# Performance work log

Hardware: AMD Instinct MI355X
Metric: run time of the kernel (lower is better)

The kernel has to match this reference:

```python
import jax, jax.numpy as jnp
import numpy as np

G, N, F, H, L, B = 8, 1024, 128, 256, 4, 64


def setup_inputs() -> dict:
    key = jax.random.key(0)
    ks = jax.random.split(key, 8)
    graph = jax.random.randint(ks[0], (B,), 0, G)
    # boolean coverpoint mask; force column 0 True so no row is empty
    mask = jax.random.uniform(ks[1], (B, N)) < 0.2
    mask = mask.at[:, 0].set(True)
    cdfg_xs = jax.random.normal(ks[2], (G, N, F), dtype=jnp.float32)
    cdfg_as = (jax.random.uniform(ks[3], (G, N, N)) < 0.02).astype(jnp.float32) / 20.0
    W_in = jax.random.normal(ks[4], (F, H), dtype=jnp.float32) * (1.0 / np.sqrt(F))
    b_in = jnp.zeros((H,), dtype=jnp.float32)
    Ws = jax.random.normal(ks[5], (L, H, H), dtype=jnp.float32) * (1.0 / np.sqrt(H))
    bs = jnp.zeros((L, H), dtype=jnp.float32)
    return {"graph": graph, "coverpoint_mask": mask, "cdfg_xs": cdfg_xs,
            "cdfg_as": cdfg_as, "W_in": W_in, "b_in": b_in, "Ws": Ws, "bs": bs}


def reference(graph, coverpoint_mask, cdfg_xs, cdfg_as, W_in, b_in, Ws, bs):
    # gather per-sample graphs (tf.gather_nd equivalent)
    xs = cdfg_xs[graph]          # [B, N, F]
    As = cdfg_as[graph]          # [B, N, N]
    # input Dense with relu
    x = jax.nn.relu(jnp.einsum('bnf,fh->bnh', xs, W_in) + b_in)  # [B, N, H]
    to_add = x
    n_layers = Ws.shape[0]
    for i in range(n_layers):
        h = jnp.einsum('bnm,bmh->bnh', As, jnp.einsum('bnh,hk->bnk', x, Ws[i])) + bs[i]
        if i == n_layers - 1:
            x = jax.nn.softmax(h, axis=-1)   # final_activation='softmax'
        else:
            x = jax.nn.relu(h)
    x = x + to_add
    # ragged boolean_mask + reduce_mean over nodes == masked mean
    m = coverpoint_mask[..., None].astype(x.dtype)   # [B, N, 1]
    s = jnp.sum(x * m, axis=1)                       # [B, H]
    cnt = jnp.maximum(jnp.sum(m, axis=1), 1.0)
    return s / cnt
```

## Files before the change

kernel.cpp:

```cpp
#include <hip/hip_runtime.h>
#include <hip/hip_bf16.h>

#define GG 8
#define NN 1024
#define FF 128
#define HH 256
#define LL 4
#define BB 64
#define MM (GG * NN)
#define ELLCAP 96

typedef __attribute__((ext_vector_type(8))) short bf16x8_t;
typedef __attribute__((ext_vector_type(4))) float f32x4_t;

__device__ inline unsigned short f2bf(float f) {
  union { float f; unsigned u; } c;
  c.f = f;
  unsigned r = (c.u + 0x7fffu + ((c.u >> 16) & 1u)) >> 16;
  return (unsigned short)r;
}
__device__ inline float bf2f(unsigned short u) {
  union { unsigned u; float f; } c;
  c.u = (unsigned)u << 16;
  return c.f;
}

__global__ void detect_mask_kernel(const uint4* __restrict__ mb,
                                   int* __restrict__ flags) {
  const int i = blockIdx.x * blockDim.x + threadIdx.x;
  const uint4 v = mb[i];
  const unsigned all = v.x | v.y | v.z | v.w;
  const int nonz = (all & 0xFFFFFF00u) != 0;
  const int isf32 = ((v.x >> 24) == 0x3fu) || ((v.y >> 24) == 0x3fu) ||
                    ((v.z >> 24) == 0x3fu) || ((v.w >> 24) == 0x3fu);
  const unsigned long long bn = __ballot(nonz);
  const unsigned long long bf = __ballot(isf32);
  if ((threadIdx.x & 63) == 0) {
    if (bn) atomicOr(&flags[0], 1);
    if (bf) atomicOr(&flags[1], 1);
  }
}

__global__ __launch_bounds__(256) void convert_xs_kernel(
    const float4* __restrict__ in, ushort4* __restrict__ out) {
  const int i = blockIdx.x * 256 + threadIdx.x;
  const float4 v = in[i];
  ushort4 o;
  o.x = f2bf(v.x); o.y = f2bf(v.y); o.z = f2bf(v.z); o.w = f2bf(v.w);
  out[i] = o;
}

__global__ __launch_bounds__(256) void convert_w_kernel(
    const float* __restrict__ W_in, const float* __restrict__ Ws,
    unsigned short* __restrict__ WinT, unsigned short* __restrict__ WsT) {
  const int idx = blockIdx.x * 256 + threadIdx.x;
  if (idx < FF * HH) {
    const int n = idx >> 7, k = idx & (FF - 1);
    WinT[idx] = f2bf(W_in[k * HH + n]);
  } else {
    const int j = idx - FF * HH;
    const int l = j >> 16, n = (j >> 8) & 255, k = j & 255;
    WsT[j] = f2bf(Ws[((size_t)l * HH + k) * HH + n]);
  }
}

__global__ __launch_bounds__(256) void ell_build_kernel(
    const float* __restrict__ Adj, uint2* __restrict__ ell,
    int* __restrict__ cntArr) {
  const int lane = threadIdx.x & 63;
  const int wid = threadIdx.x >> 6;
  const int r = blockIdx.x * 4 + wid;
  const float* __restrict__ Arow = Adj + (size_t)r * NN;
  int cnt = 0;
  for (int mc = 0; mc < NN; mc += 64) {
    const float a = Arow[mc + lane];
    const unsigned long long bal = __ballot(a != 0.0f);
    if (a != 0.0f) {
      const int pos = cnt + __popcll(bal & ((1ULL << lane) - 1ULL));
      if (pos < ELLCAP) {
        uint2 e;
        e.x = __float_as_uint(a);
        e.y = (unsigned)(mc + lane);
        ell[(size_t)r * ELLCAP + pos] = e;
      }
    }
    cnt += __popcll(bal);
  }
  if (lane == 0) cntArr[r] = min(cnt, ELLCAP);
}

template <int K, bool FUSED>
__global__ __launch_bounds__(256) void mfma_gemm_kernel(
    const unsigned short* __restrict__ A, const unsigned short* __restrict__ BT,
    const float* __restrict__ bias, unsigned short* __restrict__ Cb,
    float* __restrict__ Cf) {
  __shared__ uint4 As4[4 * 64];
  __shared__ uint4 Bs4[4 * 64];
  const int t = threadIdx.x;
  const int lane = t & 63;
  const int w = t >> 6;
  const int wm = (w >> 1) * 32;
  const int wn = (w & 1) * 32;
  const int m0 = blockIdx.x * 64;
  const int n0 = blockIdx.y * 64;
  const int srow = t >> 2;
  const int skseg = t & 3;
  const int lk = lane >> 4;
  const int lr = lane & 15;
  f32x4_t acc[2][2] = {};
  for (int k0 = 0; k0 < K; k0 += 32) {
    As4[skseg * 64 + srow] =
        *(const uint4*)(A + (size_t)(m0 + srow) * K + k0 + skseg * 8);
    Bs4[skseg * 64 + srow] =
        *(const uint4*)(BT + (size_t)(n0 + srow) * K + k0 + skseg * 8);
    __syncthreads();
    const bf16x8_t a0 = *(const bf16x8_t*)(&As4[lk * 64 + wm + lr]);
    const bf16x8_t a1 = *(const bf16x8_t*)(&As4[lk * 64 + wm + 16 + lr]);
    const bf16x8_t b0 = *(const bf16x8_t*)(&Bs4[lk * 64 + wn + lr]);
    const bf16x8_t b1 = *(const bf16x8_t*)(&Bs4[lk * 64 + wn + 16 + lr]);
    acc[0][0] = __builtin_amdgcn_mfma_f32_16x16x32_bf16(a0, b0, acc[0][0], 0, 0, 0);
    acc[0][1] = __builtin_amdgcn_mfma_f32_16x16x32_bf16(a0, b1, acc[0][1], 0, 0, 0);
    acc[1][0] = __builtin_amdgcn_mfma_f32_16x16x32_bf16(a1, b0, acc[1][0], 0, 0, 0);
    acc[1][1] = __builtin_amdgcn_mfma_f32_16x16x32_bf16(a1, b1, acc[1][1], 0, 0, 0);
    __syncthreads();
  }
#pragma unroll
  for (int rg = 0; rg < 2; ++rg)
#pragma unroll
    for (int cg = 0; cg < 2; ++cg)
#pragma unroll
      for (int j = 0; j < 4; ++j) {
        const int row = m0 + wm + rg * 16 + (lane >> 4) * 4 + j;
        const int col = n0 + wn + cg * 16 + lr;
        float v = acc[rg][cg][j];
        if (FUSED) {
          v += bias[col];
          v = fmaxf(v, 0.0f);
          Cb[(size_t)row * HH + col] = f2bf(v);
          Cf[(size_t)row * HH + col] = v;
        } else {
          Cb[(size_t)row * HH + col] = f2bf(v);
        }
      }
}

__global__ __launch_bounds__(256) void spmm_ell_kernel(
    const uint2* __restrict__ ell, const int* __restrict__ cntArr,
    const unsigned short* __restrict__ Yb, const float* __restrict__ bias,
    const float* __restrict__ X0, unsigned short* __restrict__ Xb,
    float* __restrict__ Xf, int final_layer) {
  const int lane = threadIdx.x & 63;
  const int wid = threadIdx.x >> 6;
  const int r = blockIdx.x * 4 + wid;
  const int g = r >> 10;
  const unsigned short* __restrict__ Yg = Yb + (size_t)g * NN * HH;
  const int cnt = cntArr[r];
  const uint2* __restrict__ erow = ell + (size_t)r * ELLCAP;
  float acc0 = 0.f, acc1 = 0.f, acc2 = 0.f, acc3 = 0.f;
  for (int base = 0; base < cnt; base += 64) {
    const int m = min(64, cnt - base);
    const uint2 e = erow[base + ((lane < m) ? lane : 0)];
    for (int j = 0; j < m; ++j) {
      const float v = __uint_as_float(__shfl(e.x, j));
      const int idx = (int)__shfl(e.y, j);
      const ushort4 y = *(const ushort4*)(Yg + (size_t)idx * HH + lane * 4);
      acc0 += v * bf2f(y.x);
      acc1 += v * bf2f(y.y);
      acc2 += v * bf2f(y.z);
      acc3 += v * bf2f(y.w);
    }
  }
  const float4 b4 = *(const float4*)(bias + lane * 4);
  const float h0 = acc0 + b4.x, h1 = acc1 + b4.y;
  const float h2 = acc2 + b4.z, h3 = acc3 + b4.w;
  const size_t rowoff = (size_t)r * HH;
  if (!final_layer) {
    ushort4 o;
    o.x = f2bf(fmaxf(h0, 0.f));
    o.y = f2bf(fmaxf(h1, 0.f));
    o.z = f2bf(fmaxf(h2, 0.f));
    o.w = f2bf(fmaxf(h3, 0.f));
    *(ushort4*)(Xb + rowoff + lane * 4) = o;
  } else {
    float mx = fmaxf(fmaxf(h0, h1), fmaxf(h2, h3));
#pragma unroll
    for (int off = 32; off >= 1; off >>= 1) mx = fmaxf(mx, __shfl_xor(mx, off));
    const float e0 = __expf(h0 - mx), e1 = __expf(h1 - mx);
    const float e2 = __expf(h2 - mx), e3 = __expf(h3 - mx);
    float s = e0 + e1 + e2 + e3;
#pragma unroll
    for (int off = 32; off >= 1; off >>= 1) s += __shfl_xor(s, off);
    const float inv = 1.0f / s;
    const float4 x0 = *(const float4*)(X0 + rowoff + lane * 4);
    float4 o;
    o.x = e0 * inv + x0.x;
    o.y = e1 * inv + x0.y;
    o.z = e2 * inv + x0.z;
    o.w = e3 * inv + x0.w;
    *(float4*)(Xf + rowoff + lane * 4) = o;
  }
}

__global__ __launch_bounds__(256) void mm_partial_kernel(
    const float* __restrict__ X, const int* __restrict__ graph,
    const void* __restrict__ mask, const int* __restrict__ flags,
    float* __restrict__ partial, float* __restrict__ cntbuf) {
  __shared__ unsigned char m[64];
  const int c = blockIdx.x;
  const int b = blockIdx.y;
  const int h = threadIdx.x;
  const int n0 = c * 64;
  const int mode = flags[1] ? 2 : (flags[0] ? 0 : 1);
  if (h < 64) {
    const int n = n0 + h;
    bool on;
    if (mode == 1) on = ((const int*)mask)[(size_t)b * NN + n] != 0;
    else if (mode == 2) on = ((const float*)mask)[(size_t)b * NN + n] != 0.0f;
    else on = ((const unsigned char*)mask)[(size_t)b * NN + n] != 0;
    m[h] = on ? 1 : 0;
  }
  __syncthreads();
  const int g = graph[b];
  const float* __restrict__ Xg = X + ((size_t)g * NN + n0) * HH;
  float a0 = 0.f, a1 = 0.f, a2 = 0.f, a3 = 0.f;
  int c0 = 0, c1 = 0, c2 = 0, c3 = 0;
#pragma unroll 4
  for (int n = 0; n < 16; ++n) {
    if (m[n])      { a0 += Xg[(size_t)n * HH + h]; c0++; }
    if (m[n + 16]) { a1 += Xg[(size_t)(n + 16) * HH + h]; c1++; }
    if (m[n + 32]) { a2 += Xg[(size_t)(n + 32) * HH + h]; c2++; }
    if (m[n + 48]) { a3 += Xg[(size_t)(n + 48) * HH + h]; c3++; }
  }
  partial[((size_t)b * 16 + c) * HH + h] = (a0 + a1) + (a2 + a3);
  if (h == 0) cntbuf[b * 16 + c] = (float)((c0 + c1) + (c2 + c3));
}

__global__ __launch_bounds__(256) void mm_reduce_kernel(
    const float* __restrict__ partial, const float* __restrict__ cntbuf,
    float* __restrict__ out) {
  const int b = blockIdx.x, h = threadIdx.x;
  float s = 0.f;
#pragma unroll
  for (int c = 0; c < 16; ++c) s += partial[((size_t)b * 16 + c) * HH + h];
  float cnt = 0.f;
#pragma unroll
  for (int c = 0; c < 16; ++c) cnt += cntbuf[b * 16 + c];
  out[(size_t)b * HH + h] = s / fmaxf(cnt, 1.0f);
}

extern "C" void kernel_launch(void* const* d_in, const int* in_sizes, int n_in,
                              void* d_out, int out_size, void* d_ws,
                              size_t ws_size, hipStream_t stream) {
  const int* graph = (const int*)d_in[0];
  const void* mask = d_in[1];
  const float* xs = (const float*)d_in[2];
  const float* As = (const float*)d_in[3];
  const float* W_in = (const float*)d_in[4];
  const float* b_in = (const float*)d_in[5];
  const float* Ws = (const float*)d_in[6];
  const float* bs = (const float*)d_in[7];
  float* out = (float*)d_out;

  float* X = (float*)d_ws;
  float* X0 = X + (size_t)MM * HH;
  unsigned short* Yb = (unsigned short*)(X0 + (size_t)MM * HH);
  unsigned short* Xb = Yb + (size_t)MM * HH;
  unsigned short* xsb = Xb + (size_t)MM * HH;
  unsigned short* WinT = xsb + (size_t)MM * FF;
  unsigned short* WsT = WinT + (size_t)HH * FF;
  uint2* ell = (uint2*)(WsT + (size_t)LL * HH * HH);
  int* cntArr = (int*)(ell + (size_t)MM * ELLCAP);
  int* flags = cntArr + MM;
  float* partial = (float*)(flags + 2);
  float* cntbuf = partial + (size_t)BB * 16 * HH;

  hipMemsetAsync(flags, 0, 2 * sizeof(int), stream);
  detect_mask_kernel<<<16, 256, 0, stream>>>((const uint4*)mask, flags);
  convert_xs_kernel<<<MM * FF / 4 / 256, 256, 0, stream>>>((const float4*)xs,
                                                           (ushort4*)xsb);
  convert_w_kernel<<<(FF * HH + LL * HH * HH) / 256, 256, 0, stream>>>(
      W_in, Ws, WinT, WsT);
  ell_build_kernel<<<MM / 4, 256, 0, stream>>>(As, ell, cntArr);

  const dim3 grd(MM / 64, HH / 64);
  mfma_gemm_kernel<FF, true><<<grd, 256, 0, stream>>>(xsb, WinT, b_in, Xb, X0);
  for (int i = 0; i < LL; ++i) {
    mfma_gemm_kernel<HH, false><<<grd, 256, 0, stream>>>(
        Xb, WsT + (size_t)i * HH * HH, nullptr, Yb, nullptr);
    spmm_ell_kernel<<<MM / 4, 256, 0, stream>>>(
        ell, cntArr, Yb, bs + (size_t)i * HH, X0, Xb, X, (i == LL - 1) ? 1 : 0);
  }
  mm_partial_kernel<<<dim3(16, BB), 256, 0, stream>>>(X, graph, mask, flags,
                                                      partial, cntbuf);
  mm_reduce_kernel<<<BB, 256, 0, stream>>>(partial, cntbuf, out);
}
```

Before: 209.4 us.

## Fuse prep kernels, stage full-K GEMM tiles in swizzled LDS, unroll SpMM

The four preprocessing kernels (mask detect, xs conversion, weight transpose, ELL build) are merged into one launch that dispatches work by block index. The GEMM now loads the whole K extent of each 64-row tile into XOR-swizzled shared memory once, with a single barrier, instead of a sync-heavy loop over 32-wide K slices. The SpMM inner loop is unrolled by two with split accumulators to expose more independent gather loads. The larger LDS footprint (up to 64 KB per block for K=256) may reduce occupancy.

```diff
diff --git a/kernel.cpp b/kernel.cpp
--- a/kernel.cpp
+++ b/kernel.cpp
@@ -25,68 +25,69 @@
   return c.f;
 }
 
-__global__ void detect_mask_kernel(const uint4* __restrict__ mb,
-                                   int* __restrict__ flags) {
-  const int i = blockIdx.x * blockDim.x + threadIdx.x;
-  const uint4 v = mb[i];
-  const unsigned all = v.x | v.y | v.z | v.w;
-  const int nonz = (all & 0xFFFFFF00u) != 0;
-  const int isf32 = ((v.x >> 24) == 0x3fu) || ((v.y >> 24) == 0x3fu) ||
-                    ((v.z >> 24) == 0x3fu) || ((v.w >> 24) == 0x3fu);
-  const unsigned long long bn = __ballot(nonz);
-  const unsigned long long bf = __ballot(isf32);
-  if ((threadIdx.x & 63) == 0) {
-    if (bn) atomicOr(&flags[0], 1);
-    if (bf) atomicOr(&flags[1], 1);
-  }
-}
-
-__global__ __launch_bounds__(256) void convert_xs_kernel(
-    const float4* __restrict__ in, ushort4* __restrict__ out) {
-  const int i = blockIdx.x * 256 + threadIdx.x;
-  const float4 v = in[i];
-  ushort4 o;
-  o.x = f2bf(v.x); o.y = f2bf(v.y); o.z = f2bf(v.z); o.w = f2bf(v.w);
-  out[i] = o;
-}
-
-__global__ __launch_bounds__(256) void convert_w_kernel(
+#define PB_DET 16
+#define PB_XS (PB_DET + 1024)
+#define PB_W (PB_XS + 1152)
+#define PB_ELL (PB_W + 2048)
+__global__ __launch_bounds__(256) void prep_kernel(
+    const uint4* __restrict__ mask4, int* __restrict__ flags,
+    const float4* __restrict__ xs4, ushort4* __restrict__ xsb4,
     const float* __restrict__ W_in, const float* __restrict__ Ws,
-    unsigned short* __restrict__ WinT, unsigned short* __restrict__ WsT) {
-  const int idx = blockIdx.x * 256 + threadIdx.x;
-  if (idx < FF * HH) {
-    const int n = idx >> 7, k = idx & (FF - 1);
-    WinT[idx] = f2bf(W_in[k * HH + n]);
-  } else {
-    const int j = idx - FF * HH;
-    const int l = j >> 16, n = (j >> 8) & 255, k = j & 255;
-    WsT[j] = f2bf(Ws[((size_t)l * HH + k) * HH + n]);
-  }
-}
-
-__global__ __launch_bounds__(256) void ell_build_kernel(
+    unsigned short* __restrict__ WinT, unsigned short* __restrict__ WsT,
     const float* __restrict__ Adj, uint2* __restrict__ ell,
     int* __restrict__ cntArr) {
-  const int lane = threadIdx.x & 63;
-  const int wid = threadIdx.x >> 6;
-  const int r = blockIdx.x * 4 + wid;
-  const float* __restrict__ Arow = Adj + (size_t)r * NN;
-  int cnt = 0;
-  for (int mc = 0; mc < NN; mc += 64) {
-    const float a = Arow[mc + lane];
-    const unsigned long long bal = __ballot(a != 0.0f);
-    if (a != 0.0f) {
-      const int pos = cnt + __popcll(bal & ((1ULL << lane) - 1ULL));
-      if (pos < ELLCAP) {
-        uint2 e;
-        e.x = __float_as_uint(a);
-        e.y = (unsigned)(mc + lane);
-        ell[(size_t)r * ELLCAP + pos] = e;
+  const int bx = blockIdx.x;
+  if (bx < PB_DET) {
+    const int i = bx * 256 + threadIdx.x;
+    const uint4 v = mask4[i];
+    const unsigned all = v.x | v.y | v.z | v.w;
+    const int nonz = (all & 0xFFFFFF00u) != 0;
+    const int isf32 = ((v.x >> 24) == 0x3fu) || ((v.y >> 24) == 0x3fu) ||
+                      ((v.z >> 24) == 0x3fu) || ((v.w >> 24) == 0x3fu);
+    const unsigned long long bn = __ballot(nonz);
+    const unsigned long long bf = __ballot(isf32);
+    if ((threadIdx.x & 63) == 0) {
+      if (bn) atomicOr(&flags[0], 1);
+      if (bf) atomicOr(&flags[1], 1);
+    }
+  } else if (bx < PB_XS) {
+    const int i = (bx - PB_DET) * 256 + threadIdx.x;
+    const float4 v = xs4[i];
+    ushort4 o;
+    o.x = f2bf(v.x); o.y = f2bf(v.y); o.z = f2bf(v.z); o.w = f2bf(v.w);
+    xsb4[i] = o;
+  } else if (bx < PB_W) {
+    const int idx = (bx - PB_XS) * 256 + threadIdx.x;
+    if (idx < FF * HH) {
+      const int n = idx >> 7, k = idx & (FF - 1);
+      WinT[idx] = f2bf(W_in[k * HH + n]);
+    } else {
+      const int j = idx - FF * HH;
+      const int l = j >> 16, n = (j >> 8) & 255, k = j & 255;
+      WsT[j] = f2bf(Ws[((size_t)l * HH + k) * HH + n]);
+    }
+  } else {
+    const int lane = threadIdx.x & 63;
+    const int wid = threadIdx.x >> 6;
+    const int r = (bx - PB_W) * 4 + wid;
+    const float* __restrict__ Arow = Adj + (size_t)r * NN;
+    int cnt = 0;
+    for (int mc = 0; mc < NN; mc += 64) {
+      const float a = Arow[mc + lane];
+      const unsigned long long bal = __ballot(a != 0.0f);
+      if (a != 0.0f) {
+        const int pos = cnt + __popcll(bal & ((1ULL << lane) - 1ULL));
+        if (pos < ELLCAP) {
+          uint2 e;
+          e.x = __float_as_uint(a);
+          e.y = (unsigned)(mc + lane);
+          ell[(size_t)r * ELLCAP + pos] = e;
+        }
       }
-    }
-    cnt += __popcll(bal);
-  }
-  if (lane == 0) cntArr[r] = min(cnt, ELLCAP);
+      cnt += __popcll(bal);
+    }
+    if (lane == 0) cntArr[r] = min(cnt, ELLCAP);
+  }
 }
 
 template <int K, bool FUSED>
@@ -94,8 +95,9 @@
     const unsigned short* __restrict__ A, const unsigned short* __restrict__ BT,
     const float* __restrict__ bias, unsigned short* __restrict__ Cb,
     float* __restrict__ Cf) {
-  __shared__ uint4 As4[4 * 64];
-  __shared__ uint4 Bs4[4 * 64];
+  constexpr int KS = K / 8;
+  __shared__ uint4 As4[64 * KS];
+  __shared__ uint4 Bs4[64 * KS];
   const int t = threadIdx.x;
   const int lane = t & 63;
   const int w = t >> 6;
@@ -103,26 +105,34 @@
   const int wn = (w & 1) * 32;
   const int m0 = blockIdx.x * 64;
   const int n0 = blockIdx.y * 64;
-  const int srow = t >> 2;
-  const int skseg = t & 3;
   const int lk = lane >> 4;
   const int lr = lane & 15;
+  const uint4* __restrict__ Ag = (const uint4*)(A + (size_t)m0 * K);
+  const uint4* __restrict__ Bg = (const uint4*)(BT + (size_t)n0 * K);
+#pragma unroll
+  for (int it = 0; it < K / 32; ++it) {
+    const int c = it * 256 + t;
+    const int row = c / KS;
+    const int k = c % KS;
+    const int slot = row * KS + (k ^ (row & 7));
+    As4[slot] = Ag[c];
+    Bs4[slot] = Bg[c];
+  }
+  __syncthreads();
   f32x4_t acc[2][2] = {};
-  for (int k0 = 0; k0 < K; k0 += 32) {
-    As4[skseg * 64 + srow] =
-        *(const uint4*)(A + (size_t)(m0 + srow) * K + k0 + skseg * 8);
-    Bs4[skseg * 64 + srow] =
-        *(const uint4*)(BT + (size_t)(n0 + srow) * K + k0 + skseg * 8);
-    __syncthreads();
-    const bf16x8_t a0 = *(const bf16x8_t*)(&As4[lk * 64 + wm + lr]);
-    const bf16x8_t a1 = *(const bf16x8_t*)(&As4[lk * 64 + wm + 16 + lr]);
-    const bf16x8_t b0 = *(const bf16x8_t*)(&Bs4[lk * 64 + wn + lr]);
-    const bf16x8_t b1 = *(const bf16x8_t*)(&Bs4[lk * 64 + wn + 16 + lr]);
+#pragma unroll
+  for (int ks = 0; ks < K / 32; ++ks) {
+    const int q = ks * 4 + lk;
+    const int ra0 = wm + lr, ra1 = wm + 16 + lr;
+    const int rb0 = wn + lr, rb1 = wn + 16 + lr;
+    const bf16x8_t a0 = *(const bf16x8_t*)(&As4[ra0 * KS + (q ^ (ra0 & 7))]);
+    const bf16x8_t a1 = *(const bf16x8_t*)(&As4[ra1 * KS + (q ^ (ra1 & 7))]);
+    const bf16x8_t b0 = *(const bf16x8_t*)(&Bs4[rb0 * KS + (q ^ (rb0 & 7))]);
+    const bf16x8_t b1 = *(const bf16x8_t*)(&Bs4[rb1 * KS + (q ^ (rb1 & 7))]);
     acc[0][0] = __builtin_amdgcn_mfma_f32_16x16x32_bf16(a0, b0, acc[0][0], 0, 0, 0);
     acc[0][1] = __builtin_amdgcn_mfma_f32_16x16x32_bf16(a0, b1, acc[0][1], 0, 0, 0);
     acc[1][0] = __builtin_amdgcn_mfma_f32_16x16x32_bf16(a1, b0, acc[1][0], 0, 0, 0);
     acc[1][1] = __builtin_amdgcn_mfma_f32_16x16x32_bf16(a1, b1, acc[1][1], 0, 0, 0);
-    __syncthreads();
   }
 #pragma unroll
   for (int rg = 0; rg < 2; ++rg)
@@ -156,23 +166,35 @@
   const unsigned short* __restrict__ Yg = Yb + (size_t)g * NN * HH;
   const int cnt = cntArr[r];
   const uint2* __restrict__ erow = ell + (size_t)r * ELLCAP;
-  float acc0 = 0.f, acc1 = 0.f, acc2 = 0.f, acc3 = 0.f;
+  float p0 = 0.f, p1 = 0.f, p2 = 0.f, p3 = 0.f;
+  float q0 = 0.f, q1 = 0.f, q2 = 0.f, q3 = 0.f;
   for (int base = 0; base < cnt; base += 64) {
     const int m = min(64, cnt - base);
     const uint2 e = erow[base + ((lane < m) ? lane : 0)];
-    for (int j = 0; j < m; ++j) {
-      const float v = __uint_as_float(__shfl(e.x, j));
-      const int idx = (int)__shfl(e.y, j);
-      const ushort4 y = *(const ushort4*)(Yg + (size_t)idx * HH + lane * 4);
-      acc0 += v * bf2f(y.x);
-      acc1 += v * bf2f(y.y);
-      acc2 += v * bf2f(y.z);
-      acc3 += v * bf2f(y.w);
+    int j = 0;
+    for (; j + 2 <= m; j += 2) {
+      const float v0 = __uint_as_float(__shfl(e.x, j));
+      const int i0 = (int)__shfl(e.y, j);
+      const float v1 = __uint_as_float(__shfl(e.x, j + 1));
+      const int i1 = (int)__shfl(e.y, j + 1);
+      const ushort4 y0 = *(const ushort4*)(Yg + (size_t)i0 * HH + lane * 4);
+      const ushort4 y1 = *(const ushort4*)(Yg + (size_t)i1 * HH + lane * 4);
+      p0 += v0 * bf2f(y0.x); p1 += v0 * bf2f(y0.y);
+      p2 += v0 * bf2f(y0.z); p3 += v0 * bf2f(y0.w);
+      q0 += v1 * bf2f(y1.x); q1 += v1 * bf2f(y1.y);
+      q2 += v1 * bf2f(y1.z); q3 += v1 * bf2f(y1.w);
+    }
+    if (j < m) {
+      const float v0 = __uint_as_float(__shfl(e.x, j));
+      const int i0 = (int)__shfl(e.y, j);
+      const ushort4 y0 = *(const ushort4*)(Yg + (size_t)i0 * HH + lane * 4);
+      p0 += v0 * bf2f(y0.x); p1 += v0 * bf2f(y0.y);
+      p2 += v0 * bf2f(y0.z); p3 += v0 * bf2f(y0.w);
     }
   }
   const float4 b4 = *(const float4*)(bias + lane * 4);
-  const float h0 = acc0 + b4.x, h1 = acc1 + b4.y;
-  const float h2 = acc2 + b4.z, h3 = acc3 + b4.w;
+  const float h0 = p0 + q0 + b4.x, h1 = p1 + q1 + b4.y;
+  const float h2 = p2 + q2 + b4.z, h3 = p3 + q3 + b4.w;
   const size_t rowoff = (size_t)r * HH;
   if (!final_layer) {
     ushort4 o;
@@ -275,12 +297,9 @@
   float* cntbuf = partial + (size_t)BB * 16 * HH;
 
   hipMemsetAsync(flags, 0, 2 * sizeof(int), stream);
-  detect_mask_kernel<<<16, 256, 0, stream>>>((const uint4*)mask, flags);
-  convert_xs_kernel<<<MM * FF / 4 / 256, 256, 0, stream>>>((const float4*)xs,
-                                                           (ushort4*)xsb);
-  convert_w_kernel<<<(FF * HH + LL * HH * HH) / 256, 256, 0, stream>>>(
-      W_in, Ws, WinT, WsT);
-  ell_build_kernel<<<MM / 4, 256, 0, stream>>>(As, ell, cntArr);
+  prep_kernel<<<PB_ELL, 256, 0, stream>>>(
+      (const uint4*)mask, flags, (const float4*)xs, (ushort4*)xsb, W_in, Ws,
+      WinT, WsT, As, ell, cntArr);
 
   const dim3 grd(MM / 64, HH / 64);
   mfma_gemm_kernel<FF, true><<<grd, 256, 0, stream>>>(xsb, WinT, b_in, Xb, X0);
```

Result: faster. 185.5 us (-11.4%).
